# Optimization experiments

Hardware: AMD Instinct MI355X
Metric: run time of the kernel (lower is better)

The kernel has to match this reference:

```python
import jax, jax.numpy as jnp
import numpy as np

IN_F = 512
OUT_F = 768
B = OUT_F - IN_F  # 256 discrimination features
I = 16            # intermediate features
N = 256           # batch size


def setup_inputs() -> dict:
    key = jax.random.key(0)
    kx, kT = jax.random.split(key)
    x = jax.random.normal(kx, (N, IN_F), dtype=jnp.float32)
    T = jax.random.normal(kT, (IN_F, B, I), dtype=jnp.float32) * 0.02
    return {"x": x, "T": T}


def reference(x, T):
    # M: (N, B, I) = x @ T reshaped
    M = jnp.einsum('nf,fbi->nbi', x, T)
    # pairwise L1 distance over intermediate dim: (N, N, B)
    l1 = jnp.abs(M[:, None, :, :] - M[None, :, :, :]).sum(axis=3)
    # exp-sum over the pair dim; torch sums over dim=0 of (M - M_t) where
    # M has leading unsqueeze(0) -> equivalent to summing over j here.
    out = jnp.exp(-l1).sum(axis=0) - 1.0  # (N, B); subtract self-pair
    return jnp.concatenate([x, out], axis=1)  # (N, OUT_F)
```

## Files before the change

kernel.cpp:

```cpp
#include <hip/hip_runtime.h>
#include <stdint.h>

#define IN_F 512
#define OUT_F 768
#define BD 256
#define ID 16
#define ND 256
#define CD 4096
#define MS 20

#define QSCALE 42.5f

typedef __bf16 bf16x8 __attribute__((ext_vector_type(8)));
typedef float f32x4 __attribute__((ext_vector_type(4)));

__device__ __forceinline__ unsigned short f2bf(float f) {
    union { float f; uint32_t u; } v; v.f = f;
    uint32_t u = v.u + 0x7FFFu + ((v.u >> 16) & 1u);
    return (unsigned short)(u >> 16);
}

__device__ __forceinline__ unsigned sad8(unsigned a, unsigned b, unsigned c) {
    unsigned d;
    asm("v_sad_u8 %0, %1, %2, %3" : "=v"(d) : "v"(a), "v"(b), "v"(c));
    return d;
}

__global__ __launch_bounds__(256) void xprep_kernel(const float* __restrict__ x,
                                                    unsigned short* __restrict__ xbf,
                                                    float* __restrict__ out) {
    const int bid = blockIdx.x;
    const int t = threadIdx.x;
    if (bid < 128) {
        int i0 = (bid * 256 + t) * 8;
        float4 a = *reinterpret_cast<const float4*>(x + i0);
        float4 c = *reinterpret_cast<const float4*>(x + i0 + 4);
        union { unsigned short s[8]; uint4 v; } u;
        u.s[0] = f2bf(a.x); u.s[1] = f2bf(a.y); u.s[2] = f2bf(a.z); u.s[3] = f2bf(a.w);
        u.s[4] = f2bf(c.x); u.s[5] = f2bf(c.y); u.s[6] = f2bf(c.z); u.s[7] = f2bf(c.w);
        *reinterpret_cast<uint4*>(xbf + i0) = u.v;
    } else {
        int r = (bid - 128) * 2 + (t >> 7);
        int q = t & 127;
        float4 v = reinterpret_cast<const float4*>(x + (size_t)r * IN_F)[q];
        reinterpret_cast<float4*>(out + (size_t)r * OUT_F)[q] = v;
    }
}

__global__ __launch_bounds__(1024) void mbd_fused4(const unsigned short* __restrict__ xbf,
                                                   const float* __restrict__ T,
                                                   float* __restrict__ out) {
    __shared__ __align__(16) unsigned char smem[32768 + 16384 + 4096];
    float* Tst = (float*)smem;
    float* LUT = (float*)smem;
    float* red = (float*)smem + 4096;
    unsigned short* Tfrag = (unsigned short*)(smem + 32768);
    unsigned char* Mq = smem + 32768 + 16384;

    const int b = blockIdx.x;
    const int t = threadIdx.x;
    const int lane = t & 63;
    const int w = t >> 6;
    const int rc = lane & 15;
    const int g = lane >> 4;

#pragma unroll
    for (int s = 0; s < 2; ++s) {
        int q = s * 1024 + t;
        int f = q >> 2, c4 = (q & 3) << 2;
        float4 v = *reinterpret_cast<const float4*>(T + (size_t)f * CD + b * ID + c4);
        *reinterpret_cast<float4*>(&Tst[f * ID + c4]) = v;
    }
    __syncthreads();

    {
        const int kg = t >> 4;
        const int c = t & 15;
        union { unsigned short s[8]; uint4 v; } p;
#pragma unroll
        for (int e = 0; e < 8; ++e) p.s[e] = f2bf(Tst[(kg * 8 + e) * ID + c]);
        *reinterpret_cast<uint4*>(Tfrag + (size_t)t * 8) = p.v;
    }
    __syncthreads();

    {
        const float K = -1.44269504f / QSCALE;
#pragma unroll
        for (int u = 0; u < 4; ++u) {
            int idx = t * 4 + u;
            LUT[idx] = exp2f((float)idx * K);
        }
    }

    const bf16x8* Av = reinterpret_cast<const bf16x8*>(xbf);
    const bf16x8* Bf = reinterpret_cast<const bf16x8*>(Tfrag);
    const int arow = w * 16 + rc;
    f32x4 acc = {0.f, 0.f, 0.f, 0.f};
#pragma unroll 4
    for (int k = 0; k < 16; ++k) {
        bf16x8 afr = Av[(size_t)arow * 64 + k * 4 + g];
        bf16x8 bfr = Bf[(k * 4 + g) * 16 + rc];
        acc = __builtin_amdgcn_mfma_f32_16x16x32_bf16(afr, bfr, acc, 0, 0, 0);
    }
#pragma unroll
    for (int r = 0; r < 4; ++r) {
        float q = (acc[r] + 3.0f) * QSCALE + 0.5f;
        q = fminf(fmaxf(q, 0.0f), 255.0f);
        Mq[(w * 16 + g * 4 + r) * ID + rc] = (unsigned char)(unsigned int)q;
    }
    __syncthreads();

    const uint4* Mq4 = reinterpret_cast<const uint4*>(Mq);
    uint4 ma[4];
#pragma unroll
    for (int r = 0; r < 4; ++r) ma[r] = Mq4[lane + 64 * r];

    float pacc[4] = {0.f, 0.f, 0.f, 0.f};
    const int j0 = w * 16;
#pragma unroll 4
    for (int j = j0; j < j0 + 16; ++j) {
        uint4 mb = Mq4[j];
#pragma unroll
        for (int r = 0; r < 4; ++r) {
            unsigned s = 0;
            s = sad8(ma[r].x, mb.x, s);
            s = sad8(ma[r].y, mb.y, s);
            s = sad8(ma[r].z, mb.z, s);
            s = sad8(ma[r].w, mb.w, s);
            pacc[r] += LUT[s];
        }
    }
#pragma unroll
    for (int r = 0; r < 4; ++r) red[w * ND + lane + 64 * r] = pacc[r];
    __syncthreads();

    if (t < ND) {
        float s = -1.0f;
#pragma unroll
        for (int w2 = 0; w2 < 16; ++w2) s += red[w2 * ND + t];
        out[(size_t)t * OUT_F + IN_F + b] = s;
    }
}

__global__ __launch_bounds__(256) void mbd_one(const float* __restrict__ x,
                                               const float* __restrict__ T,
                                               float* __restrict__ out) {
    __shared__ float Tsh[IN_F * ID];
    __shared__ float Msh[ND * MS];
    const int b = blockIdx.x;
    const int t = threadIdx.x;
    const int lane = t & 63;
    const int w = t >> 6;
#pragma unroll
    for (int s = 0; s < 8; ++s) {
        int q = s * 256 + t;
        int f = q >> 2, c4 = (q & 3) << 2;
        float4 v = *reinterpret_cast<const float4*>(T + (size_t)f * CD + b * ID + c4);
        *reinterpret_cast<float4*>(&Tsh[f * ID + c4]) = v;
    }
    __syncthreads();
    const int rc = lane & 15;
    const int g = lane >> 4;
    f32x4 acc[4];
#pragma unroll
    for (int i = 0; i < 4; ++i) acc[i] = f32x4{0.f, 0.f, 0.f, 0.f};
    const float* xw = x + (size_t)(w * 64 + rc) * IN_F;
    for (int k = 0; k < 16; ++k) {
        bf16x8 bfr;
#pragma unroll
        for (int e = 0; e < 8; ++e) bfr[e] = (__bf16)Tsh[(k * 32 + g * 8 + e) * ID + rc];
        const int xo = k * 32 + g * 8;
#pragma unroll
        for (int nt = 0; nt < 4; ++nt) {
            const float* ap = xw + (size_t)nt * 16 * IN_F + xo;
            float4 a0 = *reinterpret_cast<const float4*>(ap);
            float4 a1 = *reinterpret_cast<const float4*>(ap + 4);
            bf16x8 afr;
            afr[0] = (__bf16)a0.x; afr[1] = (__bf16)a0.y;
            afr[2] = (__bf16)a0.z; afr[3] = (__bf16)a0.w;
            afr[4] = (__bf16)a1.x; afr[5] = (__bf16)a1.y;
            afr[6] = (__bf16)a1.z; afr[7] = (__bf16)a1.w;
            acc[nt] = __builtin_amdgcn_mfma_f32_16x16x32_bf16(afr, bfr, acc[nt], 0, 0, 0);
        }
    }
#pragma unroll
    for (int nt = 0; nt < 4; ++nt)
#pragma unroll
        for (int r = 0; r < 4; ++r)
            Msh[((w * 4 + nt) * 16 + g * 4 + r) * MS + rc] = acc[nt][r];
    __syncthreads();
    float mr[4][ID];
#pragma unroll
    for (int r = 0; r < 4; ++r)
#pragma unroll
        for (int ii = 0; ii < 4; ++ii) {
            float4 v = *reinterpret_cast<const float4*>(&Msh[(lane + 64 * r) * MS + ii * 4]);
            mr[r][ii * 4] = v.x; mr[r][ii * 4 + 1] = v.y;
            mr[r][ii * 4 + 2] = v.z; mr[r][ii * 4 + 3] = v.w;
        }
    float pacc[4] = {0.f, 0.f, 0.f, 0.f};
    const int j0 = w * 64;
#pragma unroll 2
    for (int j = j0; j < j0 + 64; ++j) {
        float mj[ID];
#pragma unroll
        for (int ii = 0; ii < 4; ++ii) {
            float4 v = *reinterpret_cast<const float4*>(&Msh[j * MS + ii * 4]);
            mj[ii * 4] = v.x; mj[ii * 4 + 1] = v.y;
            mj[ii * 4 + 2] = v.z; mj[ii * 4 + 3] = v.w;
        }
#pragma unroll
        for (int r = 0; r < 4; ++r) {
            float s0 = 0.f, s1 = 0.f, s2 = 0.f, s3 = 0.f;
#pragma unroll
            for (int i = 0; i < ID; i += 4) {
                s0 += fabsf(mr[r][i + 0] - mj[i + 0]);
                s1 += fabsf(mr[r][i + 1] - mj[i + 1]);
                s2 += fabsf(mr[r][i + 2] - mj[i + 2]);
                s3 += fabsf(mr[r][i + 3] - mj[i + 3]);
            }
            pacc[r] += __expf(-((s0 + s1) + (s2 + s3)));
        }
    }
    float* red = Tsh;
#pragma unroll
    for (int r = 0; r < 4; ++r) red[w * 256 + lane + 64 * r] = pacc[r];
    __syncthreads();
    {
        float s = red[t] + red[256 + t] + red[512 + t] + red[768 + t] - 1.0f;
        out[(size_t)t * OUT_F + IN_F + b] = s;
    }
    if (t < IN_F / 4) {
        float4 v = reinterpret_cast<const float4*>(x + (size_t)b * IN_F)[t];
        reinterpret_cast<float4*>(out + (size_t)b * OUT_F)[t] = v;
    }
}

extern "C" void kernel_launch(void* const* d_in, const int* in_sizes, int n_in,
                              void* d_out, int out_size, void* d_ws, size_t ws_size,
                              hipStream_t stream) {
    const float* x = (const float*)d_in[0];
    const float* T = (const float*)d_in[1];
    float* out = (float*)d_out;

    const size_t needed = (size_t)ND * IN_F * 2;

    if (ws_size >= needed) {
        unsigned short* xbf = (unsigned short*)d_ws;
        xprep_kernel<<<dim3(256), dim3(256), 0, stream>>>(x, xbf, out);
        mbd_fused4<<<dim3(BD), dim3(1024), 0, stream>>>(xbf, T, out);
    } else {
        mbd_one<<<dim3(BD), dim3(256), 0, stream>>>(x, T, out);
    }
}
```

Before: 23.66 us.

## Split each feature block into two halves over rows to double grid size

The launch goes from 256 blocks to 512. Each pair of blocks shares one discrimination feature, and each block computes the pairwise SAD sums for half of the 256 rows. Each thread now handles one row over 32 partners instead of four rows over 16, and the reduction shrinks to 8 partial sums. This spreads work across more CUs on a 256-CU device, but each half-block still redoes the full T load and the MFMA projection, so that work is duplicated.

```diff
diff --git a/kernel.cpp b/kernel.cpp
--- a/kernel.cpp
+++ b/kernel.cpp
@@ -47,9 +47,9 @@
     }
 }
 
-__global__ __launch_bounds__(1024) void mbd_fused4(const unsigned short* __restrict__ xbf,
-                                                   const float* __restrict__ T,
-                                                   float* __restrict__ out) {
+__global__ __launch_bounds__(1024, 8) void mbd_fused7(const unsigned short* __restrict__ xbf,
+                                                      const float* __restrict__ T,
+                                                      float* __restrict__ out) {
     __shared__ __align__(16) unsigned char smem[32768 + 16384 + 4096];
     float* Tst = (float*)smem;
     float* LUT = (float*)smem;
@@ -57,7 +57,8 @@
     unsigned short* Tfrag = (unsigned short*)(smem + 32768);
     unsigned char* Mq = smem + 32768 + 16384;
 
-    const int b = blockIdx.x;
+    const int b = blockIdx.x >> 1;
+    const int half = blockIdx.x & 1;
     const int t = threadIdx.x;
     const int lane = t & 63;
     const int w = t >> 6;
@@ -111,34 +112,30 @@
     __syncthreads();
 
     const uint4* Mq4 = reinterpret_cast<const uint4*>(Mq);
-    uint4 ma[4];
-#pragma unroll
-    for (int r = 0; r < 4; ++r) ma[r] = Mq4[lane + 64 * r];
-
-    float pacc[4] = {0.f, 0.f, 0.f, 0.f};
-    const int j0 = w * 16;
+    const int row = t & 127;
+    const int jc = t >> 7;
+    uint4 ma = Mq4[half * 128 + row];
+
+    float pacc = 0.f;
+    const int j0 = jc * 32;
 #pragma unroll 4
-    for (int j = j0; j < j0 + 16; ++j) {
+    for (int j = j0; j < j0 + 32; ++j) {
         uint4 mb = Mq4[j];
-#pragma unroll
-        for (int r = 0; r < 4; ++r) {
-            unsigned s = 0;
-            s = sad8(ma[r].x, mb.x, s);
-            s = sad8(ma[r].y, mb.y, s);
-            s = sad8(ma[r].z, mb.z, s);
-            s = sad8(ma[r].w, mb.w, s);
-            pacc[r] += LUT[s];
-        }
-    }
-#pragma unroll
-    for (int r = 0; r < 4; ++r) red[w * ND + lane + 64 * r] = pacc[r];
-    __syncthreads();
-
-    if (t < ND) {
+        unsigned s = 0;
+        s = sad8(ma.x, mb.x, s);
+        s = sad8(ma.y, mb.y, s);
+        s = sad8(ma.z, mb.z, s);
+        s = sad8(ma.w, mb.w, s);
+        pacc += LUT[s];
+    }
+    red[t] = pacc;
+    __syncthreads();
+
+    if (t < 128) {
         float s = -1.0f;
 #pragma unroll
-        for (int w2 = 0; w2 < 16; ++w2) s += red[w2 * ND + t];
-        out[(size_t)t * OUT_F + IN_F + b] = s;
+        for (int q = 0; q < 8; ++q) s += red[q * 128 + t];
+        out[(size_t)(half * 128 + t) * OUT_F + IN_F + b] = s;
     }
 }
 
@@ -248,7 +245,7 @@
     if (ws_size >= needed) {
         unsigned short* xbf = (unsigned short*)d_ws;
         xprep_kernel<<<dim3(256), dim3(256), 0, stream>>>(x, xbf, out);
-        mbd_fused4<<<dim3(BD), dim3(1024), 0, stream>>>(xbf, T, out);
+        mbd_fused7<<<dim3(512), dim3(1024), 0, stream>>>(xbf, T, out);
     } else {
         mbd_one<<<dim3(BD), dim3(256), 0, stream>>>(x, T, out);
     }
```

After: 32.68 us. +38.2%, slower.
